# Kernel tuning notes

Measured on AMD Instinct MI355X. Metric: run time of the kernel, lower is better.

## Reference

```python
import jax, jax.numpy as jnp
import numpy as np

B, H, W = 16, 512, 512


def setup_inputs() -> dict:
    key = jax.random.key(0)
    k1, k2 = jax.random.split(key)
    roll = jax.random.normal(k1, (B,), jnp.float32) * 0.2   # radians
    pitch = jax.random.normal(k2, (B,), jnp.float32) * 0.2  # radians
    focal = jnp.full((B,), 0.7 * max(H, W), jnp.float32)    # heuristic focal (pixels)
    return {"roll": roll, "pitch": pitch, "focal": focal, "h": H, "w": W}


def _J_vecnorm(v):
    """Jacobian of v/||v|| wrt v.  v: [..., D] -> [..., D, D]."""
    n = jnp.linalg.norm(v, axis=-1, keepdims=True)[..., None]  # [...,1,1]
    n = jnp.where(n == 0, n + 1e-6, n)
    eye = jnp.eye(v.shape[-1], dtype=v.dtype)
    vvT = v[..., :, None] * v[..., None, :]
    return eye / n - vvT / n ** 3


def reference(roll, pitch, focal, h, w):
    dtype = roll.dtype
    b = roll.shape[0]

    # ---- Gravity: vec3d and Jacobian wrt (roll, pitch) ----
    sr, cr = jnp.sin(roll), jnp.cos(roll)
    sp, cp = jnp.sin(pitch), jnp.cos(pitch)
    abc = jnp.stack([-sr * cp, -cr * cp, -sp], -1)          # [B,3] unit gravity vec
    zero = jnp.zeros_like(cp)
    J_rp = jnp.stack([
        jnp.stack([-cr * cp, sr * sp], -1),
        jnp.stack([sr * cp, cr * sp], -1),
        jnp.stack([zero, -cp], -1)], -2)                     # [B,3,2]

    # ---- Pinhole camera: pixel grid, principal point, normalization ----
    ys, xs = jnp.meshgrid(jnp.arange(h, dtype=dtype) + 0.5,
                          jnp.arange(w, dtype=dtype) + 0.5, indexing="ij")
    xy = jnp.stack([xs.ravel(), ys.ravel()], -1)             # [N,2], row-major (h then w)
    c = jnp.array([w / 2.0, h / 2.0], dtype)
    f = focal[:, None, None]                                 # [B,1,1]
    uv = (xy[None] - c) / f                                  # [B,N,2]

    # ================= J_up_field =================
    c3 = abc[..., 2]
    proj = abc[:, None, :2] - c3[:, None, None] * uv         # [B,N,2] unnormalized up field
    J_norm2proj = _J_vecnorm(proj)                           # [B,N,2,2]
    zeros = jnp.zeros_like(uv[..., 0])
    ones = jnp.ones_like(zeros)
    # J of proj wrt abc: [[1,0,-u],[0,1,-v]]
    J_proj2abc = jnp.stack([
        jnp.stack([ones, zeros, -uv[..., 0]], -1),
        jnp.stack([zeros, ones, -uv[..., 1]], -1)], -2)      # [B,N,2,3]
    J_proj2delta = jnp.einsum("bnij,bjk->bnik", J_proj2abc, J_rp)      # [B,N,2,2]
    J_up2delta = jnp.einsum("bnij,bnjk->bnik", J_norm2proj, J_proj2delta)
    # J_proj2uv = -c3 * I2 ; J_uv2f (diag, summed over f-components) = -uv/f
    J_uv2f = -uv / f                                          # [B,N,2]
    J_proj2f = -c3[:, None, None] * J_uv2f                    # [B,N,2]
    J_up2f = jnp.einsum("bnij,bnj->bni", J_norm2proj, J_proj2f)[..., None]
    J_up = jnp.concatenate([J_up2delta, J_up2f], -1).reshape(b, h, w, 2, 3)

    # ================= J_latitude_field =================
    uv1 = jnp.concatenate([uv, jnp.ones_like(uv[..., :1])], -1)        # [B,N,3]
    uv1_norm = uv1 / jnp.linalg.norm(uv1, axis=-1, keepdims=True)      # bearings
    J_norm2img = _J_vecnorm(uv1)[..., :2]                               # [B,N,3,2]
    J_delta = jnp.einsum("bni,bij->bnj", uv1_norm, J_rp)               # [B,N,2]
    J_w2f = -uv / f                                                    # [B,N,2]
    J_norm2f = jnp.einsum("bnij,bnj->bni", J_norm2img, J_w2f)          # [B,N,3]
    J_f = jnp.einsum("bni,bi->bn", J_norm2f, abc)[..., None]           # [B,N,1]
    J_lat = jnp.concatenate([J_delta, J_f], -1).reshape(b, h, w, 1, 3)

    # pack (J_up [B,h,w,2,3], J_lat [B,h,w,1,3]) along the residual axis
    return jnp.concatenate([J_up, J_lat], axis=-2)            # [B,h,w,3,3]
```

## Files before the change

kernel.cpp:

```cpp
#include <hip/hip_runtime.h>

#define BB 16
#define HH 512
#define WW 512
#define PIX_PER_THREAD 4
#define THREADS_PER_BATCH ((HH * WW) / PIX_PER_THREAD)
#define TOTAL_THREADS (BB * THREADS_PER_BATCH)
#define BLOCK 256
#define F4_PER_THREAD 9
#define F4_PER_BLOCK (BLOCK * F4_PER_THREAD)

struct Px { float a00, a01, a02, a10, a11, a12, d0, d1, ff; };

__device__ __forceinline__ Px compute_px(
    float u0, float u1, float invf,
    float a0, float a1, float a2,
    float J00, float J01, float J10, float J11, float J21, float cp)
{
    const float c3 = a2;

    const float p0 = a0 - c3 * u0;
    const float p1 = a1 - c3 * u1;

    const float n2     = p0 * p0 + p1 * p1;
    const float inv_n  = rsqrtf(n2);
    const float inv_n3 = inv_n * inv_n * inv_n;
    const float M00 = inv_n - p0 * p0 * inv_n3;
    const float M01 =        -p0 * p1 * inv_n3;
    const float M11 = inv_n - p1 * p1 * inv_n3;

    const float P00 = J00;
    const float P01 = J01 + u0 * cp;
    const float P10 = J10;
    const float P11 = J11 + u1 * cp;

    Px r;
    r.a00 = M00 * P00 + M01 * P10;
    r.a01 = M00 * P01 + M01 * P11;
    r.a10 = M01 * P00 + M11 * P10;
    r.a11 = M01 * P01 + M11 * P11;

    const float q0 = c3 * u0 * invf;
    const float q1 = c3 * u1 * invf;
    r.a02 = M00 * q0 + M01 * q1;
    r.a12 = M01 * q0 + M11 * q1;

    const float nn2     = u0 * u0 + u1 * u1 + 1.0f;
    const float inv_nn  = rsqrtf(nn2);
    const float inv_nn3 = inv_nn * inv_nn * inv_nn;

    r.d0 = inv_nn * (u0 * J00 + u1 * J10);
    r.d1 = inv_nn * (u0 * J01 + u1 * J11 + J21);

    const float w0 = -u0 * invf;
    const float w1 = -u1 * invf;
    const float s  = u0 * w0 + u1 * w1;
    const float g0 = inv_nn * w0 - u0 * inv_nn3 * s;
    const float g1 = inv_nn * w1 - u1 * inv_nn3 * s;
    const float g2 =             -      inv_nn3 * s;
    r.ff = g0 * a0 + g1 * a1 + g2 * a2;

    return r;
}

__global__ __launch_bounds__(BLOCK) void jac_kernel(
    const float* __restrict__ roll,
    const float* __restrict__ pitch,
    const float* __restrict__ focal,
    float* __restrict__ out)
{
    __shared__ float4 lds4[F4_PER_BLOCK];

    const int t = blockIdx.x * BLOCK + threadIdx.x;
    const int b = t >> 16;
    const int pix0 = (t & (THREADS_PER_BATCH - 1)) * PIX_PER_THREAD;
    const int y  = pix0 >> 9;
    const int x0 = pix0 & (WW - 1);

    const float rl = roll[b];
    const float pt = pitch[b];
    const float f  = focal[b];
    const float sr = sinf(rl), cr = cosf(rl);
    const float sp = sinf(pt), cp = cosf(pt);
    const float a0 = -sr * cp, a1 = -cr * cp, a2 = -sp;
    const float J00 = -cr * cp, J01 = sr * sp;
    const float J10 =  sr * cp, J11 = cr * sp;
    const float J21 = -cp;
    const float invf = 1.0f / f;

    const float u1 = ((float)y + 0.5f - (float)HH * 0.5f) * invf;
    const float ub = ((float)x0 + 0.5f - (float)WW * 0.5f) * invf;

    const Px x = compute_px(ub,               u1, invf, a0, a1, a2, J00, J01, J10, J11, J21, cp);
    const Px y1 = compute_px(ub +        invf, u1, invf, a0, a1, a2, J00, J01, J10, J11, J21, cp);
    const Px z = compute_px(ub + 2.0f * invf, u1, invf, a0, a1, a2, J00, J01, J10, J11, J21, cp);
    const Px w = compute_px(ub + 3.0f * invf, u1, invf, a0, a1, a2, J00, J01, J10, J11, J21, cp);

    const float4 v0 = make_float4(x.a00, x.a01, x.a02, x.a10);
    const float4 v1 = make_float4(x.a11, x.a12, x.d0,  x.d1 );
    const float4 v2 = make_float4(x.ff,  y1.a00, y1.a01, y1.a02);
    const float4 v3 = make_float4(y1.a10, y1.a11, y1.a12, y1.d0);
    const float4 v4 = make_float4(y1.d1,  y1.ff,  z.a00, z.a01);
    const float4 v5 = make_float4(z.a02, z.a10, z.a11, z.a12);
    const float4 v6 = make_float4(z.d0,  z.d1,  z.ff,  w.a00);
    const float4 v7 = make_float4(w.a01, w.a02, w.a10, w.a11);
    const float4 v8 = make_float4(w.a12, w.d0,  w.d1,  w.ff);

    float4* s = &lds4[threadIdx.x * F4_PER_THREAD];
    s[0] = v0; s[1] = v1; s[2] = v2; s[3] = v3; s[4] = v4;
    s[5] = v5; s[6] = v6; s[7] = v7; s[8] = v8;

    __syncthreads();

    float4* __restrict__ ob = (float4*)out + (size_t)blockIdx.x * F4_PER_BLOCK;
#pragma unroll
    for (int k = 0; k < F4_PER_THREAD; ++k) {
        const int idx = k * BLOCK + threadIdx.x;
        ob[idx] = lds4[idx];
    }
}

extern "C" void kernel_launch(void* const* d_in, const int* in_sizes, int n_in,
                              void* d_out, int out_size, void* d_ws, size_t ws_size,
                              hipStream_t stream) {
    const float* roll  = (const float*)d_in[0];
    const float* pitch = (const float*)d_in[1];
    const float* focal = (const float*)d_in[2];
    float* out = (float*)d_out;

    dim3 grid(TOTAL_THREADS / BLOCK);
    dim3 block(BLOCK);
    jac_kernel<<<grid, block, 0, stream>>>(roll, pitch, focal, out);
}
```

Baseline: 159.7 us.

## Halve pixels per thread, use float2 LDS staging and nontemporal stores

Each thread now computes two pixels instead of four, which doubles the grid and shrinks LDS per block. Results are staged in LDS as float2 pairs and then written out with float4 nontemporal stores, with a tail branch for the leftover 128 float4s per block. The goals are higher occupancy and less cache pollution on a write-only output stream. In exchange, the trig and per-batch setup is recomputed across twice as many threads, and the nine-float2 stride may cause LDS bank conflicts.

```diff
diff --git a/kernel.cpp b/kernel.cpp
--- a/kernel.cpp
+++ b/kernel.cpp
@@ -3,12 +3,16 @@
 #define BB 16
 #define HH 512
 #define WW 512
-#define PIX_PER_THREAD 4
+#define PIX_PER_THREAD 2
 #define THREADS_PER_BATCH ((HH * WW) / PIX_PER_THREAD)
 #define TOTAL_THREADS (BB * THREADS_PER_BATCH)
 #define BLOCK 256
-#define F4_PER_THREAD 9
-#define F4_PER_BLOCK (BLOCK * F4_PER_THREAD)
+#define WORDS_PER_THREAD 18
+#define WORDS_PER_BLOCK (BLOCK * WORDS_PER_THREAD)
+#define F4_PER_BLOCK (WORDS_PER_BLOCK / 4)
+
+
+typedef float f32x4 __attribute__((ext_vector_type(4)));
 
 struct Px { float a00, a01, a02, a10, a11, a12, d0, d1, ff; };
 
@@ -69,10 +73,11 @@
     const float* __restrict__ focal,
     float* __restrict__ out)
 {
-    __shared__ float4 lds4[F4_PER_BLOCK];
+    __shared__ float2 lds2[WORDS_PER_BLOCK / 2];
 
-    const int t = blockIdx.x * BLOCK + threadIdx.x;
-    const int b = t >> 16;
+    const int tid = threadIdx.x;
+    const int t = blockIdx.x * BLOCK + tid;
+    const int b = t >> 17;
     const int pix0 = (t & (THREADS_PER_BATCH - 1)) * PIX_PER_THREAD;
     const int y  = pix0 >> 9;
     const int x0 = pix0 & (WW - 1);
@@ -88,35 +93,35 @@
     const float J21 = -cp;
     const float invf = 1.0f / f;
 
-    const float u1 = ((float)y + 0.5f - (float)HH * 0.5f) * invf;
+    const float u1 = ((float)y  + 0.5f - (float)HH * 0.5f) * invf;
     const float ub = ((float)x0 + 0.5f - (float)WW * 0.5f) * invf;
 
-    const Px x = compute_px(ub,               u1, invf, a0, a1, a2, J00, J01, J10, J11, J21, cp);
-    const Px y1 = compute_px(ub +        invf, u1, invf, a0, a1, a2, J00, J01, J10, J11, J21, cp);
-    const Px z = compute_px(ub + 2.0f * invf, u1, invf, a0, a1, a2, J00, J01, J10, J11, J21, cp);
-    const Px w = compute_px(ub + 3.0f * invf, u1, invf, a0, a1, a2, J00, J01, J10, J11, J21, cp);
+    const Px A  = compute_px(ub,        u1, invf, a0, a1, a2, J00, J01, J10, J11, J21, cp);
+    const Px Bx = compute_px(ub + invf, u1, invf, a0, a1, a2, J00, J01, J10, J11, J21, cp);
 
-    const float4 v0 = make_float4(x.a00, x.a01, x.a02, x.a10);
-    const float4 v1 = make_float4(x.a11, x.a12, x.d0,  x.d1 );
-    const float4 v2 = make_float4(x.ff,  y1.a00, y1.a01, y1.a02);
-    const float4 v3 = make_float4(y1.a10, y1.a11, y1.a12, y1.d0);
-    const float4 v4 = make_float4(y1.d1,  y1.ff,  z.a00, z.a01);
-    const float4 v5 = make_float4(z.a02, z.a10, z.a11, z.a12);
-    const float4 v6 = make_float4(z.d0,  z.d1,  z.ff,  w.a00);
-    const float4 v7 = make_float4(w.a01, w.a02, w.a10, w.a11);
-    const float4 v8 = make_float4(w.a12, w.d0,  w.d1,  w.ff);
-
-    float4* s = &lds4[threadIdx.x * F4_PER_THREAD];
-    s[0] = v0; s[1] = v1; s[2] = v2; s[3] = v3; s[4] = v4;
-    s[5] = v5; s[6] = v6; s[7] = v7; s[8] = v8;
+    float2* s = &lds2[tid * 9];
+    s[0] = make_float2(A.a00, A.a01);
+    s[1] = make_float2(A.a02, A.a10);
+    s[2] = make_float2(A.a11, A.a12);
+    s[3] = make_float2(A.d0,  A.d1 );
+    s[4] = make_float2(A.ff,  Bx.a00);
+    s[5] = make_float2(Bx.a01, Bx.a02);
+    s[6] = make_float2(Bx.a10, Bx.a11);
+    s[7] = make_float2(Bx.a12, Bx.d0);
+    s[8] = make_float2(Bx.d1,  Bx.ff);
 
     __syncthreads();
 
-    float4* __restrict__ ob = (float4*)out + (size_t)blockIdx.x * F4_PER_BLOCK;
+    const f32x4* lv = (const f32x4*)lds2;
+    f32x4* ob = (f32x4*)out + (size_t)blockIdx.x * F4_PER_BLOCK;
 #pragma unroll
-    for (int k = 0; k < F4_PER_THREAD; ++k) {
-        const int idx = k * BLOCK + threadIdx.x;
-        ob[idx] = lds4[idx];
+    for (int k = 0; k < 4; ++k) {
+        const int idx = k * BLOCK + tid;
+        __builtin_nontemporal_store(lv[idx], ob + idx);
+    }
+    if (tid < F4_PER_BLOCK - 4 * BLOCK) {
+        const int idx = 4 * BLOCK + tid;
+        __builtin_nontemporal_store(lv[idx], ob + idx);
     }
 }
 
```

New measurement: 166.9 us. 4.5% more time.
